# Kernel optimization log

Hardware: AMD Instinct MI355X
Metric: run time of the kernel (lower is better)

Reference implementation:

```python
import jax, jax.numpy as jnp
import numpy as np

HEADS = 8
EPS = 1e-12  # F.normalize default eps


def conv1x1(t, w):
    # t: (B, Cin, H, W); w: (Cout, Cin) -> (B, Cout, H, W)
    return jnp.einsum('bchw,oc->bohw', t, w)


def cosine_attn(q, k, v, scale):
    # q: (B,h,d,Nq); k,v: (B,h,d,Nk). Cosine attention: L2-normalize over feature dim d.
    q = q / jnp.maximum(jnp.linalg.norm(q, axis=2, keepdims=True), EPS)
    k = k / jnp.maximum(jnp.linalg.norm(k, axis=2, keepdims=True), EPS)
    attn = jnp.einsum('bhdq,bhdk->bhqk', q, k) * scale
    attn = jax.nn.softmax(attn, axis=-1)
    return jnp.einsum('bhqk,bhdk->bhdq', attn, v)  # (B,h,d,Nq)


def setup_inputs() -> dict:
    key = jax.random.key(0)
    ks = jax.random.split(key, 8)
    B, C, H, W, L = 8, 512, 64, 64, 16
    def w(k, o, i):
        return jax.random.normal(k, (o, i), dtype=jnp.float32) * (1.0 / np.sqrt(i))
    return {
        'x': jax.random.normal(ks[0], (B, C, H, W), dtype=jnp.float32),
        'latents': jax.random.normal(ks[1], (1, C, 1, L), dtype=jnp.float32) * 0.02,
        'w_q_lat': w(ks[2], C, C),
        'w_kv_x': w(ks[3], 2 * C, C),
        'w_q_x': w(ks[4], C, C),
        'w_kv_lat': w(ks[5], 2 * C, C),
        'w_proj': w(ks[6], C, C),
        'b_proj': jnp.zeros((C,), dtype=jnp.float32),
    }


def reference(x, latents, w_q_lat, w_kv_x, w_q_x, w_kv_lat, w_proj, b_proj):
    B, C, H, W = x.shape
    L = latents.shape[-1]
    h = HEADS
    d = C // h
    scale = d ** (-0.5)

    # latents read from spatial features (compression)
    lat = jnp.broadcast_to(latents, (B, C, 1, L))
    ql = conv1x1(lat, w_q_lat).reshape(B, h, d, L)
    kvx = conv1x1(x, w_kv_x)
    kx = kvx[:, :C].reshape(B, h, d, H * W)
    vx = kvx[:, C:].reshape(B, h, d, H * W)
    lat_read = cosine_attn(ql, kx, vx, scale).reshape(B, C, 1, L)

    # latents write back into features (expansion)
    qx = conv1x1(x, w_q_x).reshape(B, h, d, H * W)
    kvl = conv1x1(lat_read, w_kv_lat)
    kl = kvl[:, :C].reshape(B, h, d, L)
    vl = kvl[:, C:].reshape(B, h, d, L)
    x_write = cosine_attn(qx, kl, vl, scale).reshape(B, C, H, W)

    # output projection (dropout p=0 -> identity)
    return conv1x1(x_write, w_proj) + b_proj[None, :, None, None]
```

## Files before the change

kernel.cpp:

```cpp
#include <hip/hip_runtime.h>


typedef __bf16 bf16x8 __attribute__((ext_vector_type(8)));
typedef float floatx4 __attribute__((ext_vector_type(4)));
typedef short short8_t __attribute__((ext_vector_type(8)));
typedef short short4_t __attribute__((ext_vector_type(4)));

#define DEV __device__ __forceinline__

DEV float bf2f(unsigned short u){ union{unsigned int i; float f;} v; v.i = ((unsigned int)u)<<16; return v.f; }
DEV unsigned short f2bf(float f){
  __bf16 h = (__bf16)f;
  unsigned short u; __builtin_memcpy(&u, &h, 2); return u;
}

DEV void glds16(const void* g, void* l){
  __builtin_amdgcn_global_load_lds((const __attribute__((address_space(1))) void*)g,
                                   (__attribute__((address_space(3))) void*)l, 16, 0, 0);
}

#define OFF_XT     256ull
#define OFF_KVX    (OFF_XT + 33554432ull)
#define OFF_WKVX   (OFF_KVX + 67108864ull)
#define OFF_WQX    (OFF_WKVX + 1048576ull)
#define OFF_WKVL   (OFF_WQX + 524288ull)
#define OFF_WPROJ  (OFF_WKVL + 1048576ull)
#define OFF_WQLAT  (OFF_WPROJ + 524288ull)
#define OFF_LATF   (OFF_WQLAT + 524288ull)
#define OFF_BIAS   (OFF_LATF + 32768ull)
#define OFF_QLH    (OFF_BIAS + 4096ull)
#define OFF_GNUM   (OFF_QLH + 32768ull)
#define OFF_GDEN   (OFF_GNUM + 524288ull)
#define OFF_KVL    (OFF_GDEN + 4096ull)
#define OFF_KHAT   (OFF_KVL + 524288ull)
#define OFF_GVL    (OFF_KHAT + 524288ull)

__global__ void k_sniff(const unsigned short* __restrict__ x, int* flag){
  int t = threadIdx.x;
  int m = 0;
  for (int i = t; i < 4096; i += 256){ int e = (x[i]>>7)&0xFF; m = (e>m)?e:m; }
  __shared__ int red[256];
  red[t] = m; __syncthreads();
  for (int s = 128; s > 0; s >>= 1){ if (t < s) red[t] = (red[t+s]>red[t])?red[t+s]:red[t]; __syncthreads(); }
  if (t == 0) flag[0] = (red[0] > 150) ? 1 : 0;
}

__global__ __launch_bounds__(256) void k_prep(const void* s0, const void* s1, const void* s2,
                                              const void* s3, const void* s4,
                                              const void* slat, const void* sbias,
                                              unsigned short* __restrict__ wdst,
                                              float* __restrict__ latf, float* __restrict__ biasf,
                                              const int* __restrict__ flag){
  int b = blockIdx.x, t = threadIdx.x;
  int isf = *flag;
  if (b < 896){
    int e = b*2048 + t*8;
    const void* src; int off;
    if (e < 524288)      { src = s0; off = e; }
    else if (e < 786432) { src = s1; off = e - 524288; }
    else if (e < 1310720){ src = s2; off = e - 786432; }
    else if (e < 1572864){ src = s3; off = e - 1310720; }
    else                 { src = s4; off = e - 1572864; }
    if (isf){
      const float* s = (const float*)src + off;
      float4 v0 = *(const float4*)(s);
      float4 v1 = *(const float4*)(s+4);
      unsigned short tmp[8] __attribute__((aligned(16)));
      tmp[0]=f2bf(v0.x); tmp[1]=f2bf(v0.y); tmp[2]=f2bf(v0.z); tmp[3]=f2bf(v0.w);
      tmp[4]=f2bf(v1.x); tmp[5]=f2bf(v1.y); tmp[6]=f2bf(v1.z); tmp[7]=f2bf(v1.w);
      *(short8_t*)&wdst[e] = *(short8_t*)tmp;
    } else {
      *(short8_t*)&wdst[e] = *(const short8_t*)((const unsigned short*)src + off);
    }
  } else if (b < 900){
    int i = (b-896)*2048 + t*8;
#pragma unroll
    for (int j = 0; j < 8; ++j)
      latf[i+j] = isf ? ((const float*)slat)[i+j] : bf2f(((const unsigned short*)slat)[i+j]);
  } else {
    if (t < 512) biasf[t] = isf ? ((const float*)sbias)[t] : bf2f(((const unsigned short*)sbias)[t]);
  }
}

__global__ __launch_bounds__(256) void k_xt(const void* __restrict__ xraw, unsigned short* __restrict__ xT,
                                            const int* __restrict__ flag){
  int nb = blockIdx.x, cb = blockIdx.y, b = blockIdx.z;
  int n0 = nb*64, c0 = cb*64;
  __shared__ unsigned short tile[64][72];
  int t = threadIdx.x;
  if (*flag){
    const float* xp = (const float*)xraw;
#pragma unroll
    for (int i = 0; i < 4; ++i){
      int ch = i*256 + t; int c = ch>>4, n4 = (ch&15)*4;
      float4 v = *(const float4*)&xp[((size_t)(b*512 + c0 + c))*4096 + n0 + n4];
      int cc = n4 ^ (((c>>3)&7)<<3);
      tile[c][cc+0]=f2bf(v.x); tile[c][cc+1]=f2bf(v.y); tile[c][cc+2]=f2bf(v.z); tile[c][cc+3]=f2bf(v.w);
    }
  } else {
    const unsigned short* xp = (const unsigned short*)xraw;
#pragma unroll
    for (int i = 0; i < 2; ++i){
      int ch = i*256 + t; int c = ch>>3, n8 = (ch&7)*8;
      *(short8_t*)&tile[c][n8 ^ (((c>>3)&7)<<3)] =
        *(const short8_t*)&xp[((size_t)(b*512 + c0 + c))*4096 + n0 + n8];
    }
  }
  __syncthreads();
#pragma unroll
  for (int i = 0; i < 2; ++i){
    int ch = i*256 + t; int n = ch>>3, c8 = (ch&7)*8;
    unsigned short tmp[8] __attribute__((aligned(16)));
#pragma unroll
    for (int j = 0; j < 8; ++j){
      int c = c8 + j;
      tmp[j] = tile[c][n ^ (((c>>3)&7)<<3)];
    }
    *(short8_t*)&xT[((size_t)(b*4096 + n0 + n))*512 + c0 + c8] = *(short8_t*)tmp;
  }
}

__global__ __launch_bounds__(256) void k_ql(const unsigned short* __restrict__ wqlat,
                                            const float* __restrict__ latf, float* __restrict__ qlh){
  int h = blockIdx.x, o0 = h*64;
  extern __shared__ char smr[];
  float* latb = (float*)smr;
  unsigned short* wt = (unsigned short*)(smr + 8192);
  float* qbuf = (float*)(smr + 8192 + 17408);
  float* rinv = (float*)(smr + 8192 + 17408 + 4096);
  int t = threadIdx.x;
  int o = t>>2, l4 = (t&3)*4;
  float acc[4] = {0.f,0.f,0.f,0.f};
  for (int kk = 0; kk < 512; kk += 128){
    __syncthreads();
#pragma unroll
    for (int j = 0; j < 8; ++j){ int i = j*256 + t; latb[i] = latf[kk*16 + i]; }
#pragma unroll
    for (int j = 0; j < 4; ++j){ int ch = j*256 + t; int r = ch>>4, kc = (ch&15)*8;
      *(short8_t*)&wt[r*136 + kc] = *(const short8_t*)&wqlat[(size_t)(o0+r)*512 + kk + kc]; }
    __syncthreads();
    for (int k = 0; k < 128; ++k){
      float w = bf2f(wt[o*136 + k]);
      const float* lr = &latb[k*16 + l4];
#pragma unroll
      for (int j = 0; j < 4; ++j) acc[j] += w*lr[j];
    }
  }
#pragma unroll
  for (int j = 0; j < 4; ++j) qbuf[o*16 + l4 + j] = acc[j];
  __syncthreads();
  if (t < 16){
    float ss = 0.f;
    for (int oo = 0; oo < 64; ++oo){ float v = qbuf[oo*16 + t]; ss += v*v; }
    rinv[t] = 0.125f / fmaxf(sqrtf(ss), 1e-12f);
  }
  __syncthreads();
#pragma unroll
  for (int j = 0; j < 4; ++j) qlh[(h*16 + l4 + j)*64 + o] = acc[j]*rinv[l4 + j];
}

DEV void gemm128(const unsigned short* __restrict__ Ap0, const unsigned short* __restrict__ Ap1,
                 const unsigned short* __restrict__ Bp,
                 unsigned short* At, unsigned short* Bt, floatx4 (&acc)[4][4]){
  int t = threadIdx.x, lane = t&63, wave = t>>6;
  int wm = wave>>1, wn = wave&1, lr = lane&15, lq = lane>>4;
  int rsub = lane>>3;
  int koff = ((lane&7) ^ rsub)*8;
  int sw = lr&7;
  for (int kk = 0; kk < 512; kk += 64){
    __syncthreads();
#pragma unroll
    for (int c2 = 0; c2 < 4; ++c2){
      int chunk = wave*4 + c2;
      int row = chunk*8 + rsub;
      const unsigned short* gp = (chunk < 8) ? (Ap0 + (size_t)row*512 + kk + koff)
                                             : (Ap1 + (size_t)(row-64)*512 + kk + koff);
      glds16(gp, At + chunk*512);
    }
#pragma unroll
    for (int c2 = 0; c2 < 4; ++c2){
      int chunk = wave*4 + c2;
      int row = chunk*8 + rsub;
      glds16(Bp + (size_t)row*512 + kk + koff, Bt + chunk*512);
    }
    __syncthreads();
#pragma unroll
    for (int ks = 0; ks < 2; ++ks){
      int vo = ((ks*4 + lq) ^ sw)*8;
      bf16x8 a[4], b[4];
#pragma unroll
      for (int mt = 0; mt < 4; ++mt) a[mt] = *(const bf16x8*)&At[(wm*64 + mt*16 + lr)*64 + vo];
#pragma unroll
      for (int nt = 0; nt < 4; ++nt) b[nt] = *(const bf16x8*)&Bt[(wn*64 + nt*16 + lr)*64 + vo];
#pragma unroll
      for (int mt = 0; mt < 4; ++mt)
#pragma unroll
        for (int nt = 0; nt < 4; ++nt)
          acc[mt][nt] = __builtin_amdgcn_mfma_f32_16x16x32_bf16(a[mt], b[nt], acc[mt][nt], 0, 0, 0);
    }
  }
  __syncthreads();
}

__global__ __launch_bounds__(256) void k_kvattn1(const unsigned short* __restrict__ wkvx,
                                                 const unsigned short* __restrict__ xT,
                                                 const float* __restrict__ qlh2,
                                                 float* __restrict__ gnum, float* __restrict__ gden){
  int nb = blockIdx.x, h = blockIdx.y, b = blockIdx.z;
  int n0 = nb*128;
  extern __shared__ char smr[];
  unsigned short* At  = (unsigned short*)smr;
  unsigned short* Bt  = (unsigned short*)(smr + 16384);
  unsigned short* kt  = (unsigned short*)smr;
  unsigned short* vt  = (unsigned short*)(smr + 18432);
  unsigned short* qls = (unsigned short*)(smr + 35840);
  float* ssq  = (float*)(smr + 38144);
  float* wred = (float*)(smr + 38656);
  unsigned short* pt  = (unsigned short*)(smr + 38912);
  int t = threadIdx.x, lane = t&63, wave = t>>6;
  int wm = wave>>1, wn = wave&1, lr = lane&15, lq = lane>>4;
  for (int i = t; i < 1024; i += 256) qls[(i>>6)*72 + (i&63)] = f2bf(qlh2[(size_t)h*1024 + i]);
  floatx4 acc[4][4];
  floatx4 zero = {0.f,0.f,0.f,0.f};
#pragma unroll
  for (int i = 0; i < 4; ++i) for (int j = 0; j < 4; ++j) acc[i][j] = zero;
  gemm128(wkvx + (size_t)(h*64)*512, wkvx + (size_t)(512 + h*64)*512,
          xT + ((size_t)(b*4096 + n0))*512, At, Bt, acc);
  if (wm == 0){
#pragma unroll
    for (int nt = 0; nt < 4; ++nt){
      float s = 0.f;
#pragma unroll
      for (int mt = 0; mt < 4; ++mt)
#pragma unroll
        for (int r = 0; r < 4; ++r) s += acc[mt][nt][r]*acc[mt][nt][r];
      s += __shfl_xor(s, 16); s += __shfl_xor(s, 32);
      if (lq == 0) ssq[wn*64 + nt*16 + lr] = 1.f / fmaxf(sqrtf(s), 1e-12f);
    }
  } else {
#pragma unroll
    for (int mt = 0; mt < 4; ++mt)
#pragma unroll
      for (int nt = 0; nt < 4; ++nt){
        int col = wn*64 + nt*16 + lr;
#pragma unroll
        for (int r = 0; r < 4; ++r) vt[(mt*16 + lq*4 + r)*136 + col] = f2bf(acc[mt][nt][r]);
      }
  }
  __syncthreads();
  if (wm == 0){
#pragma unroll
    for (int nt = 0; nt < 4; ++nt){
      int col = wn*64 + nt*16 + lr;
      float rinv = ssq[col];
#pragma unroll
      for (int mt = 0; mt < 4; ++mt){
        unsigned short tmp[4] __attribute__((aligned(8)));
#pragma unroll
        for (int r = 0; r < 4; ++r) tmp[r] = f2bf(acc[mt][nt][r]*rinv);
        *(short4_t*)&kt[col*72 + mt*16 + lq*4] = *(short4_t*)tmp;
      }
    }
  }
  __syncthreads();
  floatx4 sl[2]; sl[0] = zero; sl[1] = zero;
#pragma unroll
  for (int ks = 0; ks < 2; ++ks){
    bf16x8 bb = *(const bf16x8*)&qls[lr*72 + ks*32 + lq*8];
#pragma unroll
    for (int i = 0; i < 2; ++i){
      bf16x8 aa = *(const bf16x8*)&kt[((wave*2 + i)*16 + lr)*72 + ks*32 + lq*8];
      sl[i] = __builtin_amdgcn_mfma_f32_16x16x32_bf16(aa, bb, sl[i], 0, 0, 0);
    }
  }
  float dp = 0.f;
  float pv[2][4];
#pragma unroll
  for (int i = 0; i < 2; ++i)
#pragma unroll
    for (int r = 0; r < 4; ++r){ float p = __expf(sl[i][r]); pv[i][r] = p; dp += p; }
  dp += __shfl_xor(dp, 16); dp += __shfl_xor(dp, 32);
  if (lq == 0) wred[wave*16 + lr] = dp;
#pragma unroll
  for (int i = 0; i < 2; ++i){
    unsigned short tmp[4] __attribute__((aligned(8)));
#pragma unroll
    for (int r = 0; r < 4; ++r) tmp[r] = f2bf(pv[i][r]);
    *(short4_t*)&pt[lr*136 + (wave*2 + i)*16 + lq*4] = *(short4_t*)tmp;
  }
  __syncthreads();
  int bh = b*8 + h;
  if (t < 16) atomicAdd(&gden[bh*16 + t], wred[t] + wred[16+t] + wred[32+t] + wred[48+t]);
  floatx4 nacc = zero;
#pragma unroll
  for (int ks = 0; ks < 4; ++ks){
    bf16x8 aa = *(const bf16x8*)&vt[(wave*16 + lr)*136 + ks*32 + lq*8];
    bf16x8 bb = *(const bf16x8*)&pt[lr*136 + ks*32 + lq*8];
    nacc = __builtin_amdgcn_mfma_f32_16x16x32_bf16(aa, bb, nacc, 0, 0, 0);
  }
  float* gp = &gnum[((size_t)bh*16 + lr)*64 + wave*16 + lq*4];
#pragma unroll
  for (int r = 0; r < 4; ++r) atomicAdd(&gp[r], nacc[r]);
}

__global__ __launch_bounds__(256) void k_kvl(const unsigned short* __restrict__ wkvl,
                                             const float* __restrict__ gnum, const float* __restrict__ gden,
                                             float* __restrict__ kvl){
  int ob = blockIdx.x, b = blockIdx.y;
  extern __shared__ char smr[];
  float* latb = (float*)smr;
  unsigned short* wt = (unsigned short*)(smr + 32768);
  int t = threadIdx.x;
  for (int i = t; i < 8192; i += 256){
    int c = i>>4, l = i&15;
    int h = c>>6, d = c&63;
    int bh = b*8 + h;
    latb[i] = gnum[((size_t)(bh*16 + l))*64 + d] / gden[bh*16 + l];
  }
  int o = t>>4, l = t&15;
  int o0 = ob*16;
  float acc = 0.f;
  for (int kk = 0; kk < 512; kk += 128){
    __syncthreads();
    { int r = t>>4, kc = (t&15)*8;
      *(short8_t*)&wt[r*136 + kc] = *(const short8_t*)&wkvl[(size_t)(o0+r)*512 + kk + kc]; }
    __syncthreads();
    for (int k = 0; k < 128; ++k) acc += bf2f(wt[o*136 + k]) * latb[(kk+k)*16 + l];
  }
  kvl[((size_t)(b*1024 + o0 + o))*16 + l] = acc;
}

__global__ void k_klnorm(const float* __restrict__ kvl, float* __restrict__ khat, float* __restrict__ gvl){
  int l = blockIdx.x, h = blockIdx.y, b = blockIdx.z, d = threadIdx.x;
  float kl = kvl[((size_t)(b*1024 + h*64 + d))*16 + l];
  float vl = kvl[((size_t)(b*1024 + 512 + h*64 + d))*16 + l];
  float ss = kl*kl;
  for (int off = 32; off; off >>= 1) ss += __shfl_xor(ss, off);
  float inv = 0.125f / fmaxf(sqrtf(ss), 1e-12f);
  size_t o = ((size_t)((b*8+h)*16 + l))*64 + d;
  khat[o] = kl*inv;
  gvl[o] = vl;
}

__global__ __launch_bounds__(256) void k_mmat(const unsigned short* __restrict__ wproj,
                                              const float* __restrict__ gvl,
                                              unsigned short* __restrict__ Mg){
  int cb = blockIdx.x, h = blockIdx.y, b = blockIdx.z;
  __shared__ unsigned short wt[128*68];
  int t = threadIdx.x;
#pragma unroll
  for (int i = 0; i < 4; ++i){ int ch = i*256 + t; int c = ch>>3, d8 = (ch&7)*8;
    *(short8_t*)&wt[c*68 + d8] = *(const short8_t*)&wproj[(size_t)(cb*128 + c)*512 + h*64 + d8]; }
  int l = t&15, cq = t>>4;
  float v[64];
  const float* vp = &gvl[((size_t)(b*8+h)*16 + l)*64];
#pragma unroll
  for (int j = 0; j < 16; ++j){ float4 f = *(const float4*)&vp[j*4];
    v[j*4+0]=f.x; v[j*4+1]=f.y; v[j*4+2]=f.z; v[j*4+3]=f.w; }
  __syncthreads();
#pragma unroll
  for (int c8 = 0; c8 < 8; ++c8){
    int c = cq*8 + c8;
    float dot = 0.f;
#pragma unroll
    for (int d = 0; d < 64; ++d) dot += bf2f(wt[c*68 + d]) * v[d];
    Mg[((size_t)(b*512) + cb*128 + c)*128 + h*16 + l] = f2bf(dot);
  }
}

__global__ __launch_bounds__(256) void k_attn2p2(const unsigned short* __restrict__ wqx,
                                                 const unsigned short* __restrict__ xT,
                                                 const float* __restrict__ khatg,
                                                 unsigned short* __restrict__ Pg){
  int nb = blockIdx.x, hp = blockIdx.y, b = blockIdx.z;
  int n0 = nb*128;
  extern __shared__ char smr[];
  unsigned short* At  = (unsigned short*)smr;
  unsigned short* Bt  = (unsigned short*)(smr + 16384);
  unsigned short* qt0 = (unsigned short*)smr;
  unsigned short* qt1 = (unsigned short*)(smr + 18432);
  unsigned short* khs = (unsigned short*)(smr + 36864);
  float* ssq = (float*)(smr + 41472);
  int t = threadIdx.x, lane = t&63, wave = t>>6;
  int wm = wave>>1, wn = wave&1, lr = lane&15, lq = lane>>4;
  for (int i = t; i < 2048; i += 256){
    int hh = i>>10, rem = i&1023;
    khs[hh*1152 + (rem>>6)*72 + (rem&63)] = f2bf(khatg[((size_t)(b*8 + hp*2 + hh))*1024 + rem]);
  }
  floatx4 acc[4][4];
  floatx4 zero = {0.f,0.f,0.f,0.f};
#pragma unroll
  for (int i = 0; i < 4; ++i) for (int j = 0; j < 4; ++j) acc[i][j] = zero;
  gemm128(wqx + (size_t)(hp*128)*512, wqx + (size_t)(hp*128 + 64)*512,
          xT + ((size_t)(b*4096 + n0))*512, At, Bt, acc);
#pragma unroll
  for (int nt = 0; nt < 4; ++nt){
    float s = 0.f;
#pragma unroll
    for (int mt = 0; mt < 4; ++mt)
#pragma unroll
      for (int r = 0; r < 4; ++r) s += acc[mt][nt][r]*acc[mt][nt][r];
    s += __shfl_xor(s, 16); s += __shfl_xor(s, 32);
    if (lq == 0) ssq[wm*128 + wn*64 + nt*16 + lr] = 1.f / fmaxf(sqrtf(s), 1e-12f);
  }
  __syncthreads();
  unsigned short* qtr = wm ? qt1 : qt0;
#pragma unroll
  for (int nt = 0; nt < 4; ++nt){
    int col = wn*64 + nt*16 + lr;
    float rinv = ssq[wm*128 + col];
#pragma unroll
    for (int mt = 0; mt < 4; ++mt){
      unsigned short tmp[4] __attribute__((aligned(8)));
#pragma unroll
      for (int r = 0; r < 4; ++r) tmp[r] = f2bf(acc[mt][nt][r]*rinv);
      *(short4_t*)&qtr[col*72 + mt*16 + lq*4] = *(short4_t*)tmp;
    }
  }
  __syncthreads();
  floatx4 sl[4];
#pragma unroll
  for (int i = 0; i < 4; ++i) sl[i] = zero;
  unsigned short* qsrc = wm ? qt1 : qt0;
#pragma unroll
  for (int ks = 0; ks < 2; ++ks){
    bf16x8 bb = *(const bf16x8*)&khs[wm*1152 + lr*72 + ks*32 + lq*8];
#pragma unroll
    for (int i = 0; i < 4; ++i){
      bf16x8 aa = *(const bf16x8*)&qsrc[((wn*4 + i)*16 + lr)*72 + ks*32 + lq*8];
      sl[i] = __builtin_amdgcn_mfma_f32_16x16x32_bf16(aa, bb, sl[i], 0, 0, 0);
    }
  }
  int h = hp*2 + wm;
#pragma unroll
  for (int i = 0; i < 4; ++i){
    float p[4], s[4];
#pragma unroll
    for (int r = 0; r < 4; ++r){ p[r] = __expf(sl[i][r]); s[r] = p[r]; }
#pragma unroll
    for (int r = 0; r < 4; ++r){
      s[r] += __shfl_xor(s[r], 1);
      s[r] += __shfl_xor(s[r], 2);
      s[r] += __shfl_xor(s[r], 4);
      s[r] += __shfl_xor(s[r], 8);
    }
    int nbase = wn*64 + i*16 + lq*4;
#pragma unroll
    for (int r = 0; r < 4; ++r)
      Pg[((size_t)(b*4096 + n0 + nbase + r))*128 + h*16 + lr] = f2bf(p[r]/s[r]);
  }
}

__global__ __launch_bounds__(256) void k_out(const unsigned short* __restrict__ Mg,
                                             const unsigned short* __restrict__ Pg,
                                             const float* __restrict__ biasf,
                                             void* __restrict__ outv, const int* __restrict__ flag){
  int nb = blockIdx.x, cb = blockIdx.y, b = blockIdx.z;
  int n0 = nb*128, c0 = cb*64;
  extern __shared__ char smr[];
  unsigned short* At = (unsigned short*)smr;
  unsigned short* Bt = At + 64*136;
  int t = threadIdx.x, lane = t&63, wave = t>>6;
  int wm = wave>>1, wn = wave&1, lr = lane&15, lq = lane>>4;
#pragma unroll
  for (int i = 0; i < 4; ++i){ int ch = i*256 + t; int r = ch>>4, p8 = (ch&15)*8;
    *(short8_t*)&At[r*136 + p8] = *(const short8_t*)&Mg[((size_t)(b*512 + c0 + r))*128 + p8]; }
#pragma unroll
  for (int i = 0; i < 8; ++i){ int ch = i*256 + t; int r = ch>>4, p8 = (ch&15)*8;
    *(short8_t*)&Bt[r*136 + p8] = *(const short8_t*)&Pg[((size_t)(b*4096 + n0 + r))*128 + p8]; }
  __syncthreads();
  floatx4 acc[2][4];
  floatx4 zero = {0.f,0.f,0.f,0.f};
#pragma unroll
  for (int i = 0; i < 2; ++i) for (int j = 0; j < 4; ++j) acc[i][j] = zero;
#pragma unroll
  for (int ks = 0; ks < 4; ++ks){
    bf16x8 a0 = *(const bf16x8*)&At[(wm*32 + lr)*136 + ks*32 + lq*8];
    bf16x8 a1 = *(const bf16x8*)&At[(wm*32 + 16 + lr)*136 + ks*32 + lq*8];
#pragma unroll
    for (int nt = 0; nt < 4; ++nt){
      bf16x8 bb = *(const bf16x8*)&Bt[(wn*64 + nt*16 + lr)*136 + ks*32 + lq*8];
      acc[0][nt] = __builtin_amdgcn_mfma_f32_16x16x32_bf16(a0, bb, acc[0][nt], 0, 0, 0);
      acc[1][nt] = __builtin_amdgcn_mfma_f32_16x16x32_bf16(a1, bb, acc[1][nt], 0, 0, 0);
    }
  }
  __syncthreads();
  float* ct = (float*)smr;
#pragma unroll
  for (int mt = 0; mt < 2; ++mt)
#pragma unroll
    for (int nt = 0; nt < 4; ++nt)
#pragma unroll
      for (int r = 0; r < 4; ++r){
        int row = wm*32 + mt*16 + lq*4 + r;
        ct[row*132 + wn*64 + nt*16 + lr] = acc[mt][nt][r] + biasf[c0 + row];
      }
  __syncthreads();
  if (*flag){
    float* of = (float*)outv;
#pragma unroll
    for (int i = 0; i < 8; ++i){ int ch = i*256 + t; int r = ch>>5, c4 = (ch&31)*4;
      *(float4*)&of[((size_t)(b*512 + c0 + r))*4096 + n0 + c4] = *(float4*)&ct[r*132 + c4]; }
  } else {
    unsigned short* ob = (unsigned short*)outv;
#pragma unroll
    for (int i = 0; i < 4; ++i){ int ch = i*256 + t; int r = ch>>4, c8 = (ch&15)*8;
      unsigned short tmp[8] __attribute__((aligned(16)));
#pragma unroll
      for (int j = 0; j < 8; ++j) tmp[j] = f2bf(ct[r*132 + c8 + j]);
      *(short8_t*)&ob[((size_t)(b*512 + c0 + r))*4096 + n0 + c8] = *(short8_t*)tmp; }
  }
}

extern "C" void kernel_launch(void* const* d_in, const int* in_sizes, int n_in,
                              void* d_out, int out_size, void* d_ws, size_t ws_size,
                              hipStream_t stream){
  (void)in_sizes; (void)n_in; (void)out_size; (void)ws_size;
  char* ws = (char*)d_ws;
  int* flag              = (int*)ws;
  unsigned short* xT     = (unsigned short*)(ws + OFF_XT);
  unsigned short* Pg     = (unsigned short*)(ws + OFF_KVX);
  unsigned short* Mg     = (unsigned short*)(ws + OFF_KVX + 8388608ull);
  unsigned short* wkvx   = (unsigned short*)(ws + OFF_WKVX);
  unsigned short* wqx    = (unsigned short*)(ws + OFF_WQX);
  unsigned short* wkvl   = (unsigned short*)(ws + OFF_WKVL);
  unsigned short* wproj  = (unsigned short*)(ws + OFF_WPROJ);
  float* latf  = (float*)(ws + OFF_LATF);
  float* biasf = (float*)(ws + OFF_BIAS);
  float* qlh   = (float*)(ws + OFF_QLH);
  float* gnum  = (float*)(ws + OFF_GNUM);
  float* gden  = (float*)(ws + OFF_GDEN);
  float* kvl   = (float*)(ws + OFF_KVL);
  float* khat  = (float*)(ws + OFF_KHAT);
  float* gvl   = (float*)(ws + OFF_GVL);

  k_sniff<<<1, 256, 0, stream>>>((const unsigned short*)d_in[0], flag);

  k_prep<<<901, 256, 0, stream>>>(d_in[3], d_in[4], d_in[5], d_in[6], d_in[2],
                                  d_in[1], d_in[7], wkvx, latf, biasf, flag);

  k_xt<<<dim3(64, 8, 8), 256, 0, stream>>>(d_in[0], xT, flag);

  k_ql<<<8, 256, 8192 + 17408 + 4096 + 64, stream>>>((unsigned short*)(ws + OFF_WQLAT), latf, qlh);

  hipMemsetAsync(ws + OFF_GNUM, 0, 524288 + 4096, stream);

  k_kvattn1<<<dim3(32, 8, 8), 256, 43264, stream>>>(wkvx, xT, qlh, gnum, gden);
  k_kvl<<<dim3(64, 8), 256, 32768 + 16*136*2, stream>>>(wkvl, gnum, gden, kvl);
  k_klnorm<<<dim3(16, 8, 8), 64, 0, stream>>>(kvl, khat, gvl);
  k_mmat<<<dim3(4, 8, 8), 256, 0, stream>>>(wproj, gvl, Mg);
  k_attn2p2<<<dim3(32, 4, 8), 256, 42496, stream>>>(wqx, xT, khat, Pg);
  k_out<<<dim3(32, 8, 8), 256, 52224, stream>>>(Mg, Pg, biasf, d_out, flag);
}
```

Measured before the change: 293.7 us.

## Double-buffer LDS tiles in shared GEMM to overlap loads with MFMA

The shared 128x128 bf16 GEMM helper now uses two LDS buffer pairs. It prefetches the next K-slice via global_load_lds while the current slice feeds the MFMAs, and needs one barrier per iteration instead of two. The aim is to hide global-load latency in the two large projection kernels. In exchange, LDS per block grows from about 43 KB to about 70 KB, which lowers the number of resident blocks per CU. The other shared-memory buffers in those kernels are moved past the new 64 KB staging area.

```diff
diff --git a/kernel.cpp b/kernel.cpp
--- a/kernel.cpp
+++ b/kernel.cpp
@@ -159,47 +159,62 @@
   for (int j = 0; j < 4; ++j) qlh[(h*16 + l4 + j)*64 + o] = acc[j]*rinv[l4 + j];
 }
 
+DEV void stage_ab(const unsigned short* __restrict__ Ap0, const unsigned short* __restrict__ Ap1,
+                  const unsigned short* __restrict__ Bp, int kk,
+                  unsigned short* At, unsigned short* Bt, int wave, int rsub, int koff){
+#pragma unroll
+  for (int c2 = 0; c2 < 4; ++c2){
+    int chunk = wave*4 + c2;
+    int row = chunk*8 + rsub;
+    const unsigned short* gp = (chunk < 8) ? (Ap0 + (size_t)row*512 + kk + koff)
+                                           : (Ap1 + (size_t)(row-64)*512 + kk + koff);
+    glds16(gp, At + chunk*512);
+  }
+#pragma unroll
+  for (int c2 = 0; c2 < 4; ++c2){
+    int chunk = wave*4 + c2;
+    int row = chunk*8 + rsub;
+    glds16(Bp + (size_t)row*512 + kk + koff, Bt + chunk*512);
+  }
+}
+
 DEV void gemm128(const unsigned short* __restrict__ Ap0, const unsigned short* __restrict__ Ap1,
                  const unsigned short* __restrict__ Bp,
-                 unsigned short* At, unsigned short* Bt, floatx4 (&acc)[4][4]){
+                 char* smr, floatx4 (&acc)[4][4]){
+  unsigned short* At0 = (unsigned short*)smr;
+  unsigned short* Bt0 = (unsigned short*)(smr + 16384);
+  unsigned short* At1 = (unsigned short*)(smr + 32768);
+  unsigned short* Bt1 = (unsigned short*)(smr + 49152);
   int t = threadIdx.x, lane = t&63, wave = t>>6;
   int wm = wave>>1, wn = wave&1, lr = lane&15, lq = lane>>4;
   int rsub = lane>>3;
   int koff = ((lane&7) ^ rsub)*8;
   int sw = lr&7;
+  stage_ab(Ap0, Ap1, Bp, 0, At0, Bt0, wave, rsub, koff);
+  __syncthreads();
   for (int kk = 0; kk < 512; kk += 64){
-    __syncthreads();
-#pragma unroll
-    for (int c2 = 0; c2 < 4; ++c2){
-      int chunk = wave*4 + c2;
-      int row = chunk*8 + rsub;
-      const unsigned short* gp = (chunk < 8) ? (Ap0 + (size_t)row*512 + kk + koff)
-                                             : (Ap1 + (size_t)(row-64)*512 + kk + koff);
-      glds16(gp, At + chunk*512);
-    }
-#pragma unroll
-    for (int c2 = 0; c2 < 4; ++c2){
-      int chunk = wave*4 + c2;
-      int row = chunk*8 + rsub;
-      glds16(Bp + (size_t)row*512 + kk + koff, Bt + chunk*512);
-    }
-    __syncthreads();
+    int cur = (kk>>6)&1;
+    unsigned short* Ac = cur ? At1 : At0;
+    unsigned short* Bc = cur ? Bt1 : Bt0;
+    if (kk < 448){
+      stage_ab(Ap0, Ap1, Bp, kk+64, cur ? At0 : At1, cur ? Bt0 : Bt1, wave, rsub, koff);
+    }
 #pragma unroll
     for (int ks = 0; ks < 2; ++ks){
       int vo = ((ks*4 + lq) ^ sw)*8;
       bf16x8 a[4], b[4];
 #pragma unroll
-      for (int mt = 0; mt < 4; ++mt) a[mt] = *(const bf16x8*)&At[(wm*64 + mt*16 + lr)*64 + vo];
-#pragma unroll
-      for (int nt = 0; nt < 4; ++nt) b[nt] = *(const bf16x8*)&Bt[(wn*64 + nt*16 + lr)*64 + vo];
+      for (int mt = 0; mt < 4; ++mt) a[mt] = *(const bf16x8*)&Ac[(wm*64 + mt*16 + lr)*64 + vo];
+#pragma unroll
+      for (int nt = 0; nt < 4; ++nt) b[nt] = *(const bf16x8*)&Bc[(wn*64 + nt*16 + lr)*64 + vo];
 #pragma unroll
       for (int mt = 0; mt < 4; ++mt)
 #pragma unroll
         for (int nt = 0; nt < 4; ++nt)
           acc[mt][nt] = __builtin_amdgcn_mfma_f32_16x16x32_bf16(a[mt], b[nt], acc[mt][nt], 0, 0, 0);
     }
-  }
-  __syncthreads();
+    __syncthreads();
+  }
 }
 
 __global__ __launch_bounds__(256) void k_kvattn1(const unsigned short* __restrict__ wkvx,
@@ -209,14 +224,12 @@
   int nb = blockIdx.x, h = blockIdx.y, b = blockIdx.z;
   int n0 = nb*128;
   extern __shared__ char smr[];
-  unsigned short* At  = (unsigned short*)smr;
-  unsigned short* Bt  = (unsigned short*)(smr + 16384);
   unsigned short* kt  = (unsigned short*)smr;
   unsigned short* vt  = (unsigned short*)(smr + 18432);
-  unsigned short* qls = (unsigned short*)(smr + 35840);
-  float* ssq  = (float*)(smr + 38144);
-  float* wred = (float*)(smr + 38656);
-  unsigned short* pt  = (unsigned short*)(smr + 38912);
+  unsigned short* pt  = (unsigned short*)(smr + 35840);
+  unsigned short* qls = (unsigned short*)(smr + 65536);
+  float* ssq  = (float*)(smr + 67840);
+  float* wred = (float*)(smr + 68352);
   int t = threadIdx.x, lane = t&63, wave = t>>6;
   int wm = wave>>1, wn = wave&1, lr = lane&15, lq = lane>>4;
   for (int i = t; i < 1024; i += 256) qls[(i>>6)*72 + (i&63)] = f2bf(qlh2[(size_t)h*1024 + i]);
@@ -225,7 +238,7 @@
 #pragma unroll
   for (int i = 0; i < 4; ++i) for (int j = 0; j < 4; ++j) acc[i][j] = zero;
   gemm128(wkvx + (size_t)(h*64)*512, wkvx + (size_t)(512 + h*64)*512,
-          xT + ((size_t)(b*4096 + n0))*512, At, Bt, acc);
+          xT + ((size_t)(b*4096 + n0))*512, smr, acc);
   if (wm == 0){
 #pragma unroll
     for (int nt = 0; nt < 4; ++nt){
@@ -375,12 +388,10 @@
   int nb = blockIdx.x, hp = blockIdx.y, b = blockIdx.z;
   int n0 = nb*128;
   extern __shared__ char smr[];
-  unsigned short* At  = (unsigned short*)smr;
-  unsigned short* Bt  = (unsigned short*)(smr + 16384);
   unsigned short* qt0 = (unsigned short*)smr;
   unsigned short* qt1 = (unsigned short*)(smr + 18432);
-  unsigned short* khs = (unsigned short*)(smr + 36864);
-  float* ssq = (float*)(smr + 41472);
+  unsigned short* khs = (unsigned short*)(smr + 65536);
+  float* ssq = (float*)(smr + 70144);
   int t = threadIdx.x, lane = t&63, wave = t>>6;
   int wm = wave>>1, wn = wave&1, lr = lane&15, lq = lane>>4;
   for (int i = t; i < 2048; i += 256){
@@ -392,7 +403,7 @@
 #pragma unroll
   for (int i = 0; i < 4; ++i) for (int j = 0; j < 4; ++j) acc[i][j] = zero;
   gemm128(wqx + (size_t)(hp*128)*512, wqx + (size_t)(hp*128 + 64)*512,
-          xT + ((size_t)(b*4096 + n0))*512, At, Bt, acc);
+          xT + ((size_t)(b*4096 + n0))*512, smr, acc);
 #pragma unroll
   for (int nt = 0; nt < 4; ++nt){
     float s = 0.f;
@@ -545,10 +556,10 @@
 
   hipMemsetAsync(ws + OFF_GNUM, 0, 524288 + 4096, stream);
 
-  k_kvattn1<<<dim3(32, 8, 8), 256, 43264, stream>>>(wkvx, xT, qlh, gnum, gden);
+  k_kvattn1<<<dim3(32, 8, 8), 256, 68608, stream>>>(wkvx, xT, qlh, gnum, gden);
   k_kvl<<<dim3(64, 8), 256, 32768 + 16*136*2, stream>>>(wkvl, gnum, gden, kvl);
   k_klnorm<<<dim3(16, 8, 8), 64, 0, stream>>>(kvl, khat, gvl);
   k_mmat<<<dim3(4, 8, 8), 256, 0, stream>>>(wproj, gvl, Mg);
-  k_attn2p2<<<dim3(32, 4, 8), 256, 42496, stream>>>(wqx, xT, khat, Pg);
+  k_attn2p2<<<dim3(32, 4, 8), 256, 71168, stream>>>(wqx, xT, khat, Pg);
   k_out<<<dim3(32, 8, 8), 256, 52224, stream>>>(Mg, Pg, biasf, d_out, flag);
 }
```

Result: no change. 288.7 us (-1.7%).
